# Kernel tuning notes

Measured on AMD Instinct MI355X. Metric: run time of the kernel, lower is better.

## Reference

```python
import jax, jax.numpy as jnp
import numpy as np

THRESHOLD = 0.5
EPS = 1e-6

def cxcywh_to_xyxy(b):
    return jnp.concatenate([b[..., :2] - b[..., 2:] / 2, b[..., :2] + b[..., 2:] / 2], axis=-1)

def xyxy_to_cxcywh(b):
    return jnp.concatenate([(b[..., :2] + b[..., 2:]) / 2, b[..., 2:] - b[..., :2]], axis=-1)

def iou_matrix(a, b, eps):
    # a: [P,4] xyxy, b: [O,4] xyxy -> [P,O]
    lb = jnp.maximum(a[:, None, :2], b[None, :, :2])
    ub = jnp.minimum(a[:, None, 2:], b[None, :, 2:])
    wh = jnp.clip(ub - lb, 0.0)
    inter = wh[..., 0] * wh[..., 1]
    area_a = (a[:, 2] - a[:, 0]) * (a[:, 3] - a[:, 1])
    area_b = (b[:, 2] - b[:, 0]) * (b[:, 3] - b[:, 1])
    union = area_a[:, None] + area_b[None, :] - inter
    return inter / (union + eps)

def match_single(priors_xyxy, t_xyxy, t_labels):
    # SSD-style matching (stand-in for Calculate_bbox_target_classes)
    n_obj = t_xyxy.shape[0]
    iou = iou_matrix(priors_xyxy, t_xyxy, EPS)          # [P,O]
    best_obj_iou = jnp.max(iou, axis=1)                 # [P]
    best_obj = jnp.argmax(iou, axis=1)                  # [P]
    best_prior = jnp.argmax(iou, axis=0)                # [O] force-match each object
    best_obj = best_obj.at[best_prior].set(jnp.arange(n_obj))
    best_obj_iou = best_obj_iou.at[best_prior].set(1.0)
    labels = t_labels[best_obj]                          # [P]
    labels = jnp.where(best_obj_iou < THRESHOLD, 0, labels)
    locs = xyxy_to_cxcywh(t_xyxy[best_obj])              # [P,4] cxcywh
    return labels, locs

def setup_inputs() -> dict:
    key = jax.random.key(0)
    k1, k2, k3, k4, k5, k6, k7 = jax.random.split(key, 7)
    B, P, C, O = 64, 8732, 81, 32
    # predictions: cxcywh-ish boxes in [0,1]
    pl_xy = jax.random.uniform(k1, (B, P, 2))
    pl_wh = jax.random.uniform(k2, (B, P, 2)) * 0.25 + 0.02
    predictlocs = jnp.concatenate([pl_xy, pl_wh], axis=-1)
    predictcls = jax.random.normal(k3, (B, P, C))
    pr_xy = jax.random.uniform(k4, (P, 2))
    pr_wh = jax.random.uniform(k5, (P, 2)) * 0.25 + 0.02
    prior_bboxes = jnp.concatenate([pr_xy, pr_wh], axis=-1)
    tb_xy = jax.random.uniform(k6, (B, O, 2)) * 0.8
    tb_wh = jax.random.uniform(k7, (B, O, 2)) * 0.2 + 0.02
    target_bboxes = jnp.concatenate([tb_xy, tb_wh], axis=-1)  # xywh
    target_labels = jax.random.randint(jax.random.fold_in(key, 99), (B, O), 1, C)
    return {"predictlocs": predictlocs, "predictcls": predictcls,
            "prior_bboxes": prior_bboxes, "target_bboxes": target_bboxes,
            "target_labels": target_labels}

def _iou_loss_masked(pred_cxcywh, tgt_cxcywh, pos_mask):
    tp = cxcywh_to_xyxy(tgt_cxcywh)
    bp = cxcywh_to_xyxy(pred_cxcywh)
    lb = jnp.maximum(tp[..., :2], bp[..., :2])
    ub = jnp.minimum(tp[..., 2:], bp[..., 2:])
    wh = jnp.clip(ub - lb, 0.0)
    inter = wh[..., 0] * wh[..., 1]
    area_b = (bp[..., 2] - bp[..., 0]) * (bp[..., 3] - bp[..., 1])
    area_t = (tp[..., 2] - tp[..., 0]) * (tp[..., 3] - tp[..., 1])
    union = area_t + area_b - inter
    v = 1.0 - inter / (union + EPS)
    n_pos = jnp.sum(pos_mask)
    return jnp.sum(jnp.where(pos_mask, v, 0.0)) / n_pos

def reference(predictlocs, predictcls, prior_bboxes, target_bboxes, target_labels):
    n_classes = predictcls.shape[2]
    # xywh -> xyxy, as in original forward
    t_xyxy = jnp.concatenate([target_bboxes[..., :2],
                              target_bboxes[..., :2] + target_bboxes[..., 2:]], axis=-1)
    priors_xyxy = cxcywh_to_xyxy(prior_bboxes)
    true_classes, true_locs = jax.vmap(match_single, in_axes=(None, 0, 0))(
        priors_xyxy, t_xyxy, target_labels)      # [B,P], [B,P,4]
    pos = true_classes != 0                       # [B,P]
    n_pos = jnp.sum(pos).astype(predictlocs.dtype)
    # IoU loss over positives (mean over positives)
    iou_loss = _iou_loss_masked(predictlocs, true_locs, pos)
    # L1 loss (mean over all elements of selected [Npos,4])
    l1 = jnp.abs(predictlocs - true_locs)
    loc_loss = jnp.sum(jnp.where(pos[..., None], l1, 0.0)) / (n_pos * 4.0)
    # CrossEntropy over all priors (mean)
    logp = jax.nn.log_softmax(predictcls.reshape(-1, n_classes), axis=-1)
    cross_loss = -jnp.mean(jnp.take_along_axis(
        logp, true_classes.reshape(-1, 1), axis=-1))
    return loc_loss, cross_loss, iou_loss
```

## Files before the change

### kernel.cpp

```cpp
#include <hip/hip_runtime.h>
#include <hip/hip_bf16.h>

#define NB 64
#define NP 8732
#define NO 32
#define NC 81
#define NROWS (NB * NP)
#define PBLK 2183


__device__ __forceinline__ float ldT(const float* p, size_t i) { return p[i]; }
__device__ __forceinline__ float ldT(const unsigned short* p, size_t i) {
    return __uint_as_float((unsigned)p[i] << 16);
}
__device__ __forceinline__ float4 ld4(const float* p, size_t i) {
    return *(const float4*)(p + i);
}
__device__ __forceinline__ float4 ld4(const unsigned short* p, size_t i) {
    ushort4 u = *(const ushort4*)(p + i);
    return make_float4(__uint_as_float((unsigned)u.x << 16),
                       __uint_as_float((unsigned)u.y << 16),
                       __uint_as_float((unsigned)u.z << 16),
                       __uint_as_float((unsigned)u.w << 16));
}

__global__ void init_kernel(const void* __restrict__ prior,
                            unsigned long long* __restrict__ bestPrior,
                            float* __restrict__ accum, int* __restrict__ flag) {
    int i = threadIdx.x;
    for (int j = i; j < NB * NO; j += blockDim.x) bestPrior[j] = 0ull;
    if (i < 4) accum[i] = 0.0f;
    if (i < 64) {
        const unsigned short* pb = (const unsigned short*)prior;
        float v = __uint_as_float((unsigned)pb[i] << 16);
        unsigned long long bad = __ballot(!(fabsf(v) <= 8.0f));
        if (i == 0) *flag = (__popcll(bad) >= 8) ? 1 : 0;
    }
}

template <typename T>
__device__ __forceinline__ void match_body(
        const T* __restrict__ prior, const T* __restrict__ tb,
        unsigned long long* __restrict__ bestPrior) {
    const int b   = blockIdx.y;
    const int o   = threadIdx.x & 31;
    const int seg = threadIdx.x >> 5;
    const int p0  = blockIdx.x * 256 + seg * 32;

    float4 t = ld4(tb, ((size_t)(b * NO + o)) * 4);
    float tx0 = t.x, ty0 = t.y, tx1 = t.x + t.z, ty1 = t.y + t.w, ta = t.z * t.w;

    float bi = -1.0f;
    int bp = 0;
    for (int j = 0; j < 32; ++j) {
        int p = p0 + j;
        if (p >= NP) break;
        float4 pr = ld4(prior, (size_t)p * 4);
        float px0 = pr.x - pr.z * 0.5f, py0 = pr.y - pr.w * 0.5f;
        float px1 = pr.x + pr.z * 0.5f, py1 = pr.y + pr.w * 0.5f;
        float pa = (px1 - px0) * (py1 - py0);
        float lbx = fmaxf(px0, tx0), lby = fmaxf(py0, ty0);
        float ubx = fminf(px1, tx1), uby = fminf(py1, ty1);
        float ww = fmaxf(ubx - lbx, 0.0f), hh = fmaxf(uby - lby, 0.0f);
        float inter = ww * hh;
        float iou = inter / (pa + ta - inter + 1e-6f);
        if (iou > bi) { bi = iou; bp = p; }
    }
    if (bi >= 0.0f) {
        unsigned long long packed =
            (((unsigned long long)__float_as_uint(bi)) << 32) | (~(unsigned)bp);
        atomicMax(&bestPrior[b * NO + o], packed);
    }
}

__global__ __launch_bounds__(256) void match_kernel(
        const void* __restrict__ prior, const void* __restrict__ tb,
        unsigned long long* __restrict__ bestPrior, const int* __restrict__ flag) {
    if (*flag)
        match_body<float>((const float*)prior, (const float*)tb, bestPrior);
    else
        match_body<unsigned short>((const unsigned short*)prior,
                                   (const unsigned short*)tb, bestPrior);
}

template <typename T>
__device__ void prepce_impl(
        const T* __restrict__ plocs, const T* __restrict__ prior,
        const T* __restrict__ tb, const int* __restrict__ tlab,
        const unsigned long long* __restrict__ bestPrior,
        const T* __restrict__ pcls, float* __restrict__ accum) {
    __shared__ float4 s_box[2][NO];
    __shared__ float  s_area[2][NO];
    __shared__ int    s_lab[2][NO];
    __shared__ unsigned s_forced[2][NO];
    __shared__ unsigned char s_lab8[256];
    __shared__ float red[4][4];

    const int tid = threadIdx.x;
    const int lane = tid & 63;
    const int wv = tid >> 6;
    const int row = blockIdx.x * 256 + tid;
    const int b = row / NP;
    const int p = row - b * NP;
    const int b0 = (blockIdx.x * 256) / NP;

    if (tid < 64) {
        int bb = tid >> 5, o = tid & 31;
        int bq = b0 + bb;
        if (bq < NB) {
            float4 t = ld4(tb, ((size_t)(bq * NO + o)) * 4);
            s_box[bb][o] = make_float4(t.x, t.y, t.x + t.z, t.y + t.w);
            s_area[bb][o] = t.z * t.w;
            s_lab[bb][o] = tlab[bq * NO + o];
            s_forced[bb][o] = ~(unsigned)(bestPrior[bq * NO + o] & 0xffffffffull);
        }
    }
    __syncthreads();

    const int bb = b - b0;
    float4 pr = ld4(prior, (size_t)p * 4);
    float px0 = pr.x - pr.z * 0.5f, py0 = pr.y - pr.w * 0.5f;
    float px1 = pr.x + pr.z * 0.5f, py1 = pr.y + pr.w * 0.5f;
    float pa = (px1 - px0) * (py1 - py0);

    float bi = -1.0f;
    int bo = 0, fo = -1;
    for (int o = 0; o < NO; ++o) {
        float4 t = s_box[bb][o];
        float lbx = fmaxf(px0, t.x), lby = fmaxf(py0, t.y);
        float ubx = fminf(px1, t.z), uby = fminf(py1, t.w);
        float ww = fmaxf(ubx - lbx, 0.0f), hh = fmaxf(uby - lby, 0.0f);
        float inter = ww * hh;
        float iou = inter / (pa + s_area[bb][o] - inter + 1e-6f);
        if (iou > bi) { bi = iou; bo = o; }
        if (s_forced[bb][o] == (unsigned)p) fo = o;
    }
    if (fo >= 0) { bo = fo; bi = 1.0f; }

    int lab = s_lab[bb][bo];
    if (bi < 0.5f) lab = 0;
    s_lab8[tid] = (unsigned char)lab;

    float l1_sum = 0.f, iou_sum = 0.f, np_sum = 0.f;
    if (lab != 0) {
        np_sum = 1.0f;
        float4 t = s_box[bb][bo];
        float x0 = t.x, y0 = t.y, x1 = t.z, y1 = t.w;
        float4 traw = ld4(tb, ((size_t)(b * NO + bo)) * 4);
        float tcx = (x0 + x1) * 0.5f, tcy = (y0 + y1) * 0.5f;
        float4 qv = ld4(plocs, (size_t)row * 4);
        l1_sum = fabsf(qv.x - tcx) + fabsf(qv.y - tcy)
               + fabsf(qv.z - traw.z) + fabsf(qv.w - traw.w);
        float qX0 = qv.x - qv.z * 0.5f, qY0 = qv.y - qv.w * 0.5f;
        float qX1 = qv.x + qv.z * 0.5f, qY1 = qv.y + qv.w * 0.5f;
        float lbx = fmaxf(x0, qX0), lby = fmaxf(y0, qY0);
        float ubx = fminf(x1, qX1), uby = fminf(y1, qY1);
        float iw = fmaxf(ubx - lbx, 0.f), ih = fmaxf(uby - lby, 0.f);
        float inter = iw * ih;
        float areaq = (qX1 - qX0) * (qY1 - qY0);
        float areat = (x1 - x0) * (y1 - y0);
        iou_sum = 1.0f - inter / (areat + areaq - inter + 1e-6f);
    }

    __syncthreads();

    const int q = lane & 15;
    const int rbase = blockIdx.x * 256;
    float c_sum = 0.f;

    #pragma unroll
    for (int i = 0; i < 8; ++i) {
        int rlA = i * 16 + wv * 4 + (lane >> 4);
        int rlB = rlA + 128;
        int labA = s_lab8[rlA];
        int labB = s_lab8[rlB];
        const T* xrA = pcls + (size_t)(rbase + rlA) * NC;
        const T* xrB = pcls + (size_t)(rbase + rlB) * NC;

        float vA[5], vB[5];
        #pragma unroll
        for (int j = 0; j < 5; ++j) { vA[j] = ldT(xrA, q + 16 * j);
                                      vB[j] = ldT(xrB, q + 16 * j); }
        float v80A = (q == 0) ? ldT(xrA, 80) : -1e30f;
        float v80B = (q == 0) ? ldT(xrB, 80) : -1e30f;
        float xlA = (q == 0) ? ldT(xrA, labA) : 0.f;
        float xlB = (q == 0) ? ldT(xrB, labB) : 0.f;

        float mA = fmaxf(fmaxf(fmaxf(vA[0], vA[1]), fmaxf(vA[2], vA[3])),
                         fmaxf(vA[4], v80A));
        float mB = fmaxf(fmaxf(fmaxf(vB[0], vB[1]), fmaxf(vB[2], vB[3])),
                         fmaxf(vB[4], v80B));
        #pragma unroll
        for (int d = 1; d < 16; d <<= 1) {
            mA = fmaxf(mA, __shfl_xor(mA, d));
            mB = fmaxf(mB, __shfl_xor(mB, d));
        }
        float sA = __expf(vA[0] - mA) + __expf(vA[1] - mA) + __expf(vA[2] - mA)
                 + __expf(vA[3] - mA) + __expf(vA[4] - mA) + __expf(v80A - mA);
        float sB = __expf(vB[0] - mB) + __expf(vB[1] - mB) + __expf(vB[2] - mB)
                 + __expf(vB[3] - mB) + __expf(vB[4] - mB) + __expf(v80B - mB);
        #pragma unroll
        for (int d = 1; d < 16; d <<= 1) {
            sA += __shfl_xor(sA, d);
            sB += __shfl_xor(sB, d);
        }
        if (q == 0) {
            c_sum += (mA + __logf(sA)) - xlA;
            c_sum += (mB + __logf(sB)) - xlB;
        }
    }

    #pragma unroll
    for (int d = 1; d < 64; d <<= 1) {
        c_sum   += __shfl_xor(c_sum, d);
        l1_sum  += __shfl_xor(l1_sum, d);
        iou_sum += __shfl_xor(iou_sum, d);
        np_sum  += __shfl_xor(np_sum, d);
    }
    if (lane == 0) {
        red[wv][0] = c_sum; red[wv][1] = l1_sum;
        red[wv][2] = iou_sum; red[wv][3] = np_sum;
    }
    __syncthreads();
    if (tid == 0) {
        float a0 = 0, a1 = 0, a2 = 0, a3 = 0;
        for (int k = 0; k < 4; ++k) {
            a0 += red[k][0]; a1 += red[k][1]; a2 += red[k][2]; a3 += red[k][3];
        }
        atomicAdd(&accum[0], a0);
        atomicAdd(&accum[1], a1);
        atomicAdd(&accum[2], a2);
        atomicAdd(&accum[3], a3);
    }
}

__global__ __launch_bounds__(256) void prepce_kernel(
        const void* __restrict__ plocs, const void* __restrict__ prior,
        const void* __restrict__ tb, const int* __restrict__ tlab,
        const unsigned long long* __restrict__ bestPrior,
        const void* __restrict__ pcls,
        const int* __restrict__ flag, float* __restrict__ accum) {
    if (*flag)
        prepce_impl<float>((const float*)plocs, (const float*)prior,
                           (const float*)tb, tlab, bestPrior,
                           (const float*)pcls, accum);
    else
        prepce_impl<unsigned short>((const unsigned short*)plocs,
                                    (const unsigned short*)prior,
                                    (const unsigned short*)tb,
                                    tlab, bestPrior,
                                    (const unsigned short*)pcls, accum);
}

__global__ void finalize_kernel(const float* __restrict__ accum,
                                const int* __restrict__ flag, void* __restrict__ out) {
    if (threadIdx.x == 0) {
        float cross = accum[0] / (float)NROWS;
        float npos = accum[3];
        float loc = accum[1] / (npos * 4.0f);
        float iou = accum[2] / npos;
        if (*flag) {
            float* o = (float*)out;
            o[0] = loc; o[1] = cross; o[2] = iou;
        } else {
            __hip_bfloat16* o = (__hip_bfloat16*)out;
            o[0] = __float2bfloat16(loc);
            o[1] = __float2bfloat16(cross);
            o[2] = __float2bfloat16(iou);
        }
    }
}

extern "C" void kernel_launch(void* const* d_in, const int* in_sizes, int n_in,
                              void* d_out, int out_size, void* d_ws, size_t ws_size,
                              hipStream_t stream) {
    const void* plocs = d_in[0];
    const void* pcls  = d_in[1];
    const void* prior = d_in[2];
    const void* tb    = d_in[3];
    const int*  tlab  = (const int*)d_in[4];

    char* w = (char*)d_ws;
    unsigned long long* bestPrior = (unsigned long long*)w;
    float* accum = (float*)(w + 16384);
    int*   flag  = (int*)(w + 16400);

    hipLaunchKernelGGL(init_kernel, dim3(1), dim3(256), 0, stream,
                       prior, bestPrior, accum, flag);

    dim3 gA((NP + 255) / 256, NB);
    hipLaunchKernelGGL(match_kernel, gA, dim3(256), 0, stream,
                       prior, tb, bestPrior, flag);

    hipLaunchKernelGGL(prepce_kernel, dim3(PBLK), dim3(256), 0, stream,
                       plocs, prior, tb, tlab, bestPrior, pcls, flag, accum);

    hipLaunchKernelGGL(finalize_kernel, dim3(1), dim3(64), 0, stream,
                       accum, flag, d_out);
}
```

Baseline: 375.1 us.

## Process four CE rows per iteration with DPP row reductions

```diff
diff --git a/kernel.cpp b/kernel.cpp
--- a/kernel.cpp
+++ b/kernel.cpp
@@ -23,6 +23,18 @@
                        __uint_as_float((unsigned)u.z << 16),
                        __uint_as_float((unsigned)u.w << 16));
 }
+
+template <int CTRL>
+__device__ __forceinline__ float dppf(float x) {
+    return __int_as_float(__builtin_amdgcn_update_dpp(
+        0, __float_as_int(x), CTRL, 0xF, 0xF, true));
+}
+#define DPP_RED16(var, OP)                      \
+    var = OP(var, dppf<0x128>(var));            \
+    var = OP(var, dppf<0x124>(var));            \
+    var = OP(var, dppf<0x122>(var));            \
+    var = OP(var, dppf<0x121>(var));
+__device__ __forceinline__ float addf(float a, float b) { return a + b; }
 
 __global__ void init_kernel(const void* __restrict__ prior,
                             unsigned long long* __restrict__ bestPrior,
@@ -125,6 +137,7 @@
 
     float bi = -1.0f;
     int bo = 0, fo = -1;
+    #pragma unroll 8
     for (int o = 0; o < NO; ++o) {
         float4 t = s_box[bb][o];
         float lbx = fmaxf(px0, t.x), lby = fmaxf(py0, t.y);
@@ -165,48 +178,55 @@
     __syncthreads();
 
     const int q = lane & 15;
+    const int g = wv * 4 + (lane >> 4);
     const int rbase = blockIdx.x * 256;
     float c_sum = 0.f;
 
     #pragma unroll
-    for (int i = 0; i < 8; ++i) {
-        int rlA = i * 16 + wv * 4 + (lane >> 4);
-        int rlB = rlA + 128;
-        int labA = s_lab8[rlA];
-        int labB = s_lab8[rlB];
-        const T* xrA = pcls + (size_t)(rbase + rlA) * NC;
-        const T* xrB = pcls + (size_t)(rbase + rlB) * NC;
-
-        float vA[5], vB[5];
-        #pragma unroll
-        for (int j = 0; j < 5; ++j) { vA[j] = ldT(xrA, q + 16 * j);
-                                      vB[j] = ldT(xrB, q + 16 * j); }
-        float v80A = (q == 0) ? ldT(xrA, 80) : -1e30f;
-        float v80B = (q == 0) ? ldT(xrB, 80) : -1e30f;
-        float xlA = (q == 0) ? ldT(xrA, labA) : 0.f;
-        float xlB = (q == 0) ? ldT(xrB, labB) : 0.f;
-
-        float mA = fmaxf(fmaxf(fmaxf(vA[0], vA[1]), fmaxf(vA[2], vA[3])),
-                         fmaxf(vA[4], v80A));
-        float mB = fmaxf(fmaxf(fmaxf(vB[0], vB[1]), fmaxf(vB[2], vB[3])),
-                         fmaxf(vB[4], v80B));
-        #pragma unroll
-        for (int d = 1; d < 16; d <<= 1) {
-            mA = fmaxf(mA, __shfl_xor(mA, d));
-            mB = fmaxf(mB, __shfl_xor(mB, d));
-        }
-        float sA = __expf(vA[0] - mA) + __expf(vA[1] - mA) + __expf(vA[2] - mA)
-                 + __expf(vA[3] - mA) + __expf(vA[4] - mA) + __expf(v80A - mA);
-        float sB = __expf(vB[0] - mB) + __expf(vB[1] - mB) + __expf(vB[2] - mB)
-                 + __expf(vB[3] - mB) + __expf(vB[4] - mB) + __expf(v80B - mB);
-        #pragma unroll
-        for (int d = 1; d < 16; d <<= 1) {
-            sA += __shfl_xor(sA, d);
-            sB += __shfl_xor(sB, d);
+    for (int i = 0; i < 4; ++i) {
+        const T* xr[4];
+        int labv[4];
+        float v[4][5], v80[4], xl[4], m[4], sm[4];
+
+        #pragma unroll
+        for (int s = 0; s < 4; ++s) {
+            int rl = i * 16 + g + s * 64;
+            labv[s] = s_lab8[rl];
+            xr[s] = pcls + (size_t)(rbase + rl) * NC;
+        }
+        #pragma unroll
+        for (int s = 0; s < 4; ++s) {
+            #pragma unroll
+            for (int j = 0; j < 5; ++j) v[s][j] = ldT(xr[s], q + 16 * j);
+        }
+        #pragma unroll
+        for (int s = 0; s < 4; ++s) {
+            v80[s] = -1e30f; xl[s] = 0.f;
+            if (q == 0) {
+                v80[s] = ldT(xr[s], 80);
+                xl[s] = labv[s] ? ldT(xr[s], labv[s]) : v[s][0];
+            }
+        }
+        #pragma unroll
+        for (int s = 0; s < 4; ++s) {
+            float mm = fmaxf(fmaxf(fmaxf(v[s][0], v[s][1]),
+                                   fmaxf(v[s][2], v[s][3])),
+                             fmaxf(v[s][4], v80[s]));
+            DPP_RED16(mm, fmaxf)
+            m[s] = mm;
+        }
+        #pragma unroll
+        for (int s = 0; s < 4; ++s) {
+            float ss = __expf(v[s][0] - m[s]) + __expf(v[s][1] - m[s])
+                     + __expf(v[s][2] - m[s]) + __expf(v[s][3] - m[s])
+                     + __expf(v[s][4] - m[s]) + __expf(v80[s] - m[s]);
+            DPP_RED16(ss, addf)
+            sm[s] = ss;
         }
         if (q == 0) {
-            c_sum += (mA + __logf(sA)) - xlA;
-            c_sum += (mB + __logf(sB)) - xlB;
+            #pragma unroll
+            for (int s = 0; s < 4; ++s)
+                c_sum += (m[s] + __logf(sm[s])) - xl[s];
         }
     }
 
@@ -234,7 +254,7 @@
     }
 }
 
-__global__ __launch_bounds__(256) void prepce_kernel(
+__global__ __launch_bounds__(256, 4) void prepce_kernel(
         const void* __restrict__ plocs, const void* __restrict__ prior,
         const void* __restrict__ tb, const int* __restrict__ tlab,
         const unsigned long long* __restrict__ bestPrior,
```

Result: no change. 370.1 us (-1.3%).
